# Kernel tuning notes

Hardware: AMD Instinct MI355X
Metric: run time of the kernel (lower is better)

Reference implementation:

```python
import jax, jax.numpy as jnp
import numpy as np

B, IN, H = 8192, 1024, 1024


def setup_inputs() -> dict:
    key = jax.random.key(0)
    ks = jax.random.split(key, 12)
    s_in = 1.0 / np.sqrt(IN + H)  # torch Linear default init scale
    inp = {
        "x": jax.random.normal(ks[0], (B, IN), jnp.float32),
        "h_prev": jax.random.normal(ks[1], (B, H), jnp.float32),
        "c_prev": jax.random.normal(ks[2], (B, H), jnp.float32),
        "embed": jax.random.normal(ks[3], (B, H), jnp.float32),
    }
    for i, g in enumerate(("forget", "input", "update", "out")):
        inp[f"W_{g}"] = jax.random.uniform(ks[4 + 2 * i], (IN + H, H), jnp.float32, -s_in, s_in)
        inp[f"b_{g}"] = jax.random.uniform(ks[5 + 2 * i], (H,), jnp.float32, -s_in, s_in)
    return inp


def reference(x, h_prev, c_prev, embed,
              W_forget, b_forget, W_input, b_input,
              W_update, b_update, W_out, b_out):
    # cat_input: [B, IN+H]; embed is accepted but unused (matches source forward)
    cat_input = jnp.concatenate((x.reshape(x.shape[0], -1), h_prev), axis=1)
    # Fuse the 4 gate GEMMs into one [B, IN+H] x [IN+H, 4H] matmul (same math)
    W = jnp.concatenate((W_forget, W_input, W_update, W_out), axis=1)  # [IN+H, 4H]
    b = jnp.concatenate((b_forget, b_input, b_update, b_out))          # [4H]
    gates = cat_input @ W + b                                          # [B, 4H]
    f_t, i_t, g_t, o_t = jnp.split(gates, 4, axis=1)
    f_t = jax.nn.sigmoid(f_t)
    i_t = jax.nn.sigmoid(i_t)
    c_opt = jnp.tanh(g_t)
    c_t = c_prev * f_t + i_t * c_opt
    o_t = jax.nn.sigmoid(o_t)
    h_t = o_t * jnp.tanh(c_t)
    return (h_t, c_t)
```

## Files before the change

### kernel.cpp

```cpp
#include <hip/hip_runtime.h>
#include <hip/hip_bf16.h>


typedef __attribute__((ext_vector_type(8))) short short8;
typedef __attribute__((ext_vector_type(4))) float f32x4;

#define GLOBAL_AS __attribute__((address_space(1)))
#define LDS_AS    __attribute__((address_space(3)))

__device__ __forceinline__ void load_lds16(const void* g, void* l) {
  __builtin_amdgcn_global_load_lds((const GLOBAL_AS unsigned int*)g,
                                   (LDS_AS unsigned int*)l, 16, 0, 0);
}

__device__ __forceinline__ unsigned short f2bf(float f) {
  unsigned int u = __float_as_uint(f);
  return (unsigned short)((u + 0x7FFFu + ((u >> 16) & 1u)) >> 16);
}
__device__ __forceinline__ float sigf(float x) { return 1.0f / (1.0f + __expf(-x)); }
__device__ __forceinline__ float tanh_fast(float x) {
  return 1.0f - 2.0f / (__expf(2.0f * x) + 1.0f);
}

__global__ void pack_kernel(const float* __restrict__ x,
                            const float* __restrict__ h,
                            const float* __restrict__ W0,
                            const float* __restrict__ W1,
                            const float* __restrict__ W2,
                            const float* __restrict__ W3,
                            unsigned short* __restrict__ Apk,
                            unsigned short* __restrict__ Wp) {
  int blk = blockIdx.x;
  if (blk < 8192) {
    int t = blk * 256 + threadIdx.x;
    int row = t >> 8;
    int c   = t & 255;
    int k   = c << 3;
    const float* src = (k < 1024) ? (x + (size_t)row * 1024 + k)
                                  : (h + (size_t)row * 1024 + (k - 1024));
    float4 f0 = ((const float4*)src)[0];
    float4 f1 = ((const float4*)src)[1];
    union { unsigned short us[8]; uint4 v; } u;
    u.us[0] = f2bf(f0.x); u.us[1] = f2bf(f0.y);
    u.us[2] = f2bf(f0.z); u.us[3] = f2bf(f0.w);
    u.us[4] = f2bf(f1.x); u.us[5] = f2bf(f1.y);
    u.us[6] = f2bf(f1.z); u.us[7] = f2bf(f1.w);
    *(uint4*)(Apk + (size_t)row * 2048 + c * 8) = u.v;
  } else {
    int b  = blk - 8192;
    int c  = b & 255;
    int nb = (b >> 8) & 3;
    int g  = b >> 10;
    const float* Wg = (g == 0) ? W0 : (g == 1) ? W1 : (g == 2) ? W2 : W3;
    int np = nb * 256 + threadIdx.x;
    int kbase = c << 3;
    union { unsigned short us[8]; uint4 v; } u;
#pragma unroll
    for (int j = 0; j < 8; ++j)
      u.us[j] = f2bf(Wg[(size_t)(kbase + j) * 1024 + np]);
    int n = (g << 10) + np;
    *(uint4*)(Wp + (size_t)n * 2048 + c * 8) = u.v;
  }
}

#define MFMA16(va, vb, vc) __builtin_amdgcn_mfma_f32_16x16x32_bf16(va, vb, vc, 0, 0, 0)

__global__ __launch_bounds__(512, 2) void lstm_gemm_kernel(
    const unsigned short* __restrict__ Apk,
    const unsigned short* __restrict__ Wp,
    const float* __restrict__ c_prev,
    const float* __restrict__ bF, const float* __restrict__ bI,
    const float* __restrict__ bU, const float* __restrict__ bO,
    float* __restrict__ outH, float* __restrict__ outC) {
  extern __shared__ unsigned short LDSu[];

  const int tid = threadIdx.x;
  const int l   = tid & 63;
  const int wv  = tid >> 6;
  const int wr  = wv >> 2;
  const int wc  = wv & 3;

  int bid = blockIdx.x;
  int wg  = ((bid & 7) << 6) | (bid >> 3);
  const int mblk = wg >> 4;
  const int nblk = wg & 15;
  const int brow = mblk << 8;

  const int rl  = l & 15;
  const int cg  = l >> 4;
  const int sc  = cg ^ ((rl >> 1) & 3);
  const int aRdBase = (wr * 128 + rl) * 32 + sc * 8;
  const int bRdBase = (wc * 64 + rl) * 32 + sc * 8;

  const int srow = wv * 16 + (l >> 2);
  const int csw  = ((l & 3) ^ ((l >> 3) & 3)) * 8;
  const unsigned short* aSrc0 = Apk + (size_t)(brow + srow) * 2048 + csw;
  const unsigned short* aSrc1 = aSrc0 + (size_t)128 * 2048;
  int p0 = nblk * 256 + srow;
  int n0 = (((p0 >> 4) & 3) << 10) | ((p0 >> 6) << 4) | (p0 & 15);
  int p1 = p0 + 128;
  int n1 = (((p1 >> 4) & 3) << 10) | ((p1 >> 6) << 4) | (p1 & 15);
  const unsigned short* bSrc0 = Wp + (size_t)n0 * 2048 + csw;
  const unsigned short* bSrc1 = Wp + (size_t)n1 * 2048 + csw;

  f32x4 acc[8][4];
#pragma unroll
  for (int m = 0; m < 8; ++m)
#pragma unroll
    for (int g = 0; g < 4; ++g) acc[m][g] = (f32x4)0.0f;

#pragma unroll
  for (int s = 0; s < 3; ++s) {
    const int pb = s * 8192;
    const int so = s * 32;
    load_lds16(aSrc0 + so, &LDSu[pb + wv * 512]);
    load_lds16(aSrc1 + so, &LDSu[pb + 4096 + wv * 512]);
    load_lds16(bSrc0 + so, &LDSu[32768 + pb + wv * 512]);
    load_lds16(bSrc1 + so, &LDSu[32768 + pb + 4096 + wv * 512]);
  }
  asm volatile("s_waitcnt vmcnt(8)");
  __builtin_amdgcn_s_barrier();

#pragma unroll 1
  for (int s = 0; s < 64; ++s) {
    const int ring  = (s & 3) * 8192;
    const int pring = ((s + 3) & 3) * 8192;
    int sp = s + 3; sp = sp > 63 ? 63 : sp;
    const int so = sp * 32;
    load_lds16(aSrc0 + so, &LDSu[pring + wv * 512]);
    load_lds16(aSrc1 + so, &LDSu[pring + 4096 + wv * 512]);
    load_lds16(bSrc0 + so, &LDSu[32768 + pring + wv * 512]);
    load_lds16(bSrc1 + so, &LDSu[32768 + pring + 4096 + wv * 512]);

    short8 bfr[4], afr[8];
#pragma unroll
    for (int g = 0; g < 4; ++g)
      bfr[g] = *(const short8*)&LDSu[32768 + ring + bRdBase + g * 512];
#pragma unroll
    for (int m = 0; m < 8; ++m)
      afr[m] = *(const short8*)&LDSu[ring + aRdBase + m * 512];

    __builtin_amdgcn_s_setprio(1);
#pragma unroll
    for (int m = 0; m < 8; ++m)
#pragma unroll
      for (int g = 0; g < 4; ++g)
        acc[m][g] = MFMA16(afr[m], bfr[g], acc[m][g]);
    __builtin_amdgcn_s_setprio(0);

    asm volatile("s_waitcnt vmcnt(8)");
    __builtin_amdgcn_s_barrier();
  }

  const int colh = nblk * 64 + wc * 16 + rl;
  const float biasF = bF[colh], biasI = bI[colh];
  const float biasU = bU[colh], biasO = bO[colh];
  const int row0 = brow + wr * 128 + ((l >> 4) << 2);
#pragma unroll
  for (int m = 0; m < 8; ++m) {
#pragma unroll
    for (int r = 0; r < 4; ++r) {
      int row = row0 + m * 16 + r;
      size_t idx = (size_t)row * 1024 + colh;
      float f  = sigf(acc[m][0][r] + biasF);
      float i_ = sigf(acc[m][1][r] + biasI);
      float g_ = tanh_fast(acc[m][2][r] + biasU);
      float o_ = sigf(acc[m][3][r] + biasO);
      float cp = c_prev[idx];
      float cn = cp * f + i_ * g_;
      outH[idx] = o_ * tanh_fast(cn);
      outC[idx] = cn;
    }
  }
}

extern "C" void kernel_launch(void* const* d_in, const int* in_sizes, int n_in,
                              void* d_out, int out_size, void* d_ws, size_t ws_size,
                              hipStream_t stream) {
  const float* x      = (const float*)d_in[0];
  const float* h_prev = (const float*)d_in[1];
  const float* c_prev = (const float*)d_in[2];
  const float* Wf = (const float*)d_in[4];
  const float* bf = (const float*)d_in[5];
  const float* Wi = (const float*)d_in[6];
  const float* bi = (const float*)d_in[7];
  const float* Wu = (const float*)d_in[8];
  const float* bu = (const float*)d_in[9];
  const float* Wo = (const float*)d_in[10];
  const float* bo = (const float*)d_in[11];

  unsigned short* Apk = (unsigned short*)d_ws;
  unsigned short* Wp  = (unsigned short*)((char*)d_ws + (size_t)8192 * 2048 * 2);

  pack_kernel<<<12288, 256, 0, stream>>>(x, h_prev, Wf, Wi, Wu, Wo, Apk, Wp);

  hipFuncSetAttribute((const void*)lstm_gemm_kernel,
                      hipFuncAttributeMaxDynamicSharedMemorySize, 131072);

  float* outH = (float*)d_out;
  float* outC = outH + (size_t)8192 * 1024;
  lstm_gemm_kernel<<<512, 512, 131072, stream>>>(Apk, Wp, c_prev,
                                                 bf, bi, bu, bo, outH, outC);
}
```

Before: 183.9 us.

## Load B fragments straight from global into registers, keep only A in LDS

The weight (B) operand no longer goes through LDS. Each wave now loads its own B fragments from global memory into registers, double-buffered one K-step ahead. Only the A tiles stay in the LDS ring, so shared memory shrinks to a 64 KB static allocation, and the A fragment reads are split into two halves to save registers. This removes the LDS write/read traffic for B and its share of the barrier. In exchange, waves that share B columns load the same data redundantly, global-load latency is hidden by only one step, and the compiler's automatic waits on the register loads may serialize the A prefetch.

```diff
diff --git a/kernel.cpp b/kernel.cpp
--- a/kernel.cpp
+++ b/kernel.cpp
@@ -65,6 +65,50 @@
 
 #define MFMA16(va, vb, vc) __builtin_amdgcn_mfma_f32_16x16x32_bf16(va, vb, vc, 0, 0, 0)
 
+#define SLOT(S, BCUR, BNXT)                                                    \
+  {                                                                            \
+    const int ring_ = ((S) & 3) * 8192;                                        \
+    {                                                                          \
+      int sn_ = (S) + 1; sn_ = sn_ > 63 ? 63 : sn_;                            \
+      _Pragma("unroll")                                                        \
+      for (int gg = 0; gg < 4; ++gg)                                           \
+        BNXT[gg] = *(const short8*)(bSrcG[gg] + sn_ * 32);                     \
+    }                                                                          \
+    {                                                                          \
+      int sp_ = (S) + 3; sp_ = sp_ > 63 ? 63 : sp_;                            \
+      const int pr_ = ((S) + 3) & 3;                                           \
+      load_lds16(aSrc0 + sp_ * 32, &LDSu[pr_ * 8192 + wv * 512]);              \
+      load_lds16(aSrc1 + sp_ * 32, &LDSu[pr_ * 8192 + 4096 + wv * 512]);       \
+    }                                                                          \
+    {                                                                          \
+      short8 av[4];                                                            \
+      _Pragma("unroll")                                                        \
+      for (int mm = 0; mm < 4; ++mm)                                           \
+        av[mm] = *(const short8*)&LDSu[ring_ + aRdBase + mm * 512];            \
+      __builtin_amdgcn_s_setprio(1);                                           \
+      _Pragma("unroll")                                                        \
+      for (int mm = 0; mm < 4; ++mm) {                                         \
+        _Pragma("unroll")                                                      \
+        for (int gg = 0; gg < 4; ++gg)                                         \
+          acc[mm][gg] = MFMA16(av[mm], BCUR[gg], acc[mm][gg]);                 \
+      }                                                                        \
+      __builtin_amdgcn_s_setprio(0);                                           \
+      _Pragma("unroll")                                                        \
+      for (int mm = 0; mm < 4; ++mm)                                           \
+        av[mm] = *(const short8*)&LDSu[ring_ + aRdBase + (4 + mm) * 512];      \
+      __builtin_amdgcn_s_setprio(1);                                           \
+      _Pragma("unroll")                                                        \
+      for (int mm = 0; mm < 4; ++mm) {                                         \
+        _Pragma("unroll")                                                      \
+        for (int gg = 0; gg < 4; ++gg)                                         \
+          acc[4 + mm][gg] = MFMA16(av[mm], BCUR[gg], acc[4 + mm][gg]);         \
+      }                                                                        \
+      __builtin_amdgcn_s_setprio(0);                                           \
+    }                                                                          \
+    asm volatile("s_waitcnt vmcnt(4)");                                        \
+    __builtin_amdgcn_s_barrier();                                              \
+  }
+
 __global__ __launch_bounds__(512, 2) void lstm_gemm_kernel(
     const unsigned short* __restrict__ Apk,
     const unsigned short* __restrict__ Wp,
@@ -72,7 +116,7 @@
     const float* __restrict__ bF, const float* __restrict__ bI,
     const float* __restrict__ bU, const float* __restrict__ bO,
     float* __restrict__ outH, float* __restrict__ outC) {
-  extern __shared__ unsigned short LDSu[];
+  __shared__ __align__(16) unsigned short LDSu[32768];
 
   const int tid = threadIdx.x;
   const int l   = tid & 63;
@@ -90,18 +134,19 @@
   const int cg  = l >> 4;
   const int sc  = cg ^ ((rl >> 1) & 3);
   const int aRdBase = (wr * 128 + rl) * 32 + sc * 8;
-  const int bRdBase = (wc * 64 + rl) * 32 + sc * 8;
 
   const int srow = wv * 16 + (l >> 2);
   const int csw  = ((l & 3) ^ ((l >> 3) & 3)) * 8;
   const unsigned short* aSrc0 = Apk + (size_t)(brow + srow) * 2048 + csw;
   const unsigned short* aSrc1 = aSrc0 + (size_t)128 * 2048;
-  int p0 = nblk * 256 + srow;
-  int n0 = (((p0 >> 4) & 3) << 10) | ((p0 >> 6) << 4) | (p0 & 15);
-  int p1 = p0 + 128;
-  int n1 = (((p1 >> 4) & 3) << 10) | ((p1 >> 6) << 4) | (p1 & 15);
-  const unsigned short* bSrc0 = Wp + (size_t)n0 * 2048 + csw;
-  const unsigned short* bSrc1 = Wp + (size_t)n1 * 2048 + csw;
+
+  const unsigned short* bSrcG[4];
+#pragma unroll
+  for (int g = 0; g < 4; ++g) {
+    int p = nblk * 256 + wc * 64 + g * 16 + rl;
+    int n = (((p >> 4) & 3) << 10) | ((p >> 6) << 4) | (p & 15);
+    bSrcG[g] = Wp + (size_t)n * 2048 + cg * 8;
+  }
 
   f32x4 acc[8][4];
 #pragma unroll
@@ -109,47 +154,24 @@
 #pragma unroll
     for (int g = 0; g < 4; ++g) acc[m][g] = (f32x4)0.0f;
 
+  short8 bEven[4], bOdd[4];
+
+#pragma unroll
+  for (int g = 0; g < 4; ++g)
+    bEven[g] = *(const short8*)(bSrcG[g] + 0);
 #pragma unroll
   for (int s = 0; s < 3; ++s) {
-    const int pb = s * 8192;
-    const int so = s * 32;
-    load_lds16(aSrc0 + so, &LDSu[pb + wv * 512]);
-    load_lds16(aSrc1 + so, &LDSu[pb + 4096 + wv * 512]);
-    load_lds16(bSrc0 + so, &LDSu[32768 + pb + wv * 512]);
-    load_lds16(bSrc1 + so, &LDSu[32768 + pb + 4096 + wv * 512]);
-  }
-  asm volatile("s_waitcnt vmcnt(8)");
+    load_lds16(aSrc0 + s * 32, &LDSu[s * 8192 + wv * 512]);
+    load_lds16(aSrc1 + s * 32, &LDSu[s * 8192 + 4096 + wv * 512]);
+  }
+  asm volatile("s_waitcnt vmcnt(4)");
   __builtin_amdgcn_s_barrier();
 
 #pragma unroll 1
-  for (int s = 0; s < 64; ++s) {
-    const int ring  = (s & 3) * 8192;
-    const int pring = ((s + 3) & 3) * 8192;
-    int sp = s + 3; sp = sp > 63 ? 63 : sp;
-    const int so = sp * 32;
-    load_lds16(aSrc0 + so, &LDSu[pring + wv * 512]);
-    load_lds16(aSrc1 + so, &LDSu[pring + 4096 + wv * 512]);
-    load_lds16(bSrc0 + so, &LDSu[32768 + pring + wv * 512]);
-    load_lds16(bSrc1 + so, &LDSu[32768 + pring + 4096 + wv * 512]);
-
-    short8 bfr[4], afr[8];
-#pragma unroll
-    for (int g = 0; g < 4; ++g)
-      bfr[g] = *(const short8*)&LDSu[32768 + ring + bRdBase + g * 512];
-#pragma unroll
-    for (int m = 0; m < 8; ++m)
-      afr[m] = *(const short8*)&LDSu[ring + aRdBase + m * 512];
-
-    __builtin_amdgcn_s_setprio(1);
-#pragma unroll
-    for (int m = 0; m < 8; ++m)
-#pragma unroll
-      for (int g = 0; g < 4; ++g)
-        acc[m][g] = MFMA16(afr[m], bfr[g], acc[m][g]);
-    __builtin_amdgcn_s_setprio(0);
-
-    asm volatile("s_waitcnt vmcnt(8)");
-    __builtin_amdgcn_s_barrier();
+  for (int u = 0; u < 32; ++u) {
+    const int s0 = 2 * u;
+    SLOT(s0,     bEven, bOdd)
+    SLOT(s0 + 1, bOdd,  bEven)
   }
 
   const int colh = nblk * 64 + wc * 16 + rl;
@@ -194,11 +216,8 @@
 
   pack_kernel<<<12288, 256, 0, stream>>>(x, h_prev, Wf, Wi, Wu, Wo, Apk, Wp);
 
-  hipFuncSetAttribute((const void*)lstm_gemm_kernel,
-                      hipFuncAttributeMaxDynamicSharedMemorySize, 131072);
-
   float* outH = (float*)d_out;
   float* outC = outH + (size_t)8192 * 1024;
-  lstm_gemm_kernel<<<512, 512, 131072, stream>>>(Apk, Wp, c_prev,
-                                                 bf, bi, bu, bo, outH, outC);
-}
+  lstm_gemm_kernel<<<512, 512, 0, stream>>>(Apk, Wp, c_prev,
+                                            bf, bi, bu, bo, outH, outC);
+}
```

New measurement: 247.3 us. 1.34x slower.

## Shrink GEMM tile to 128x128 with 3-stage ring and more blocks

Applied to the files above, without the earlier changes.

The block tile shrinks from 256x256 (512 threads) to 128x128 (256 threads, 2x2 waves). The grid becomes 2048 blocks with static 48KB LDS and a 3-slot prefetch ring unrolled by three, so ring indices are compile-time constants. The aim is higher occupancy (3 blocks per CU) and better load balance across CUs. The cost is lower arithmetic intensity per block, which means more global and L2 traffic for the same work.

```diff
diff --git a/kernel.cpp b/kernel.cpp
--- a/kernel.cpp
+++ b/kernel.cpp
@@ -65,99 +65,103 @@
 
 #define MFMA16(va, vb, vc) __builtin_amdgcn_mfma_f32_16x16x32_bf16(va, vb, vc, 0, 0, 0)
 
-__global__ __launch_bounds__(512, 2) void lstm_gemm_kernel(
+#define SLOT3(S, RR, PR)                                                       \
+  {                                                                            \
+    int sp_ = (S) + 2; sp_ = sp_ > 63 ? 63 : sp_;                              \
+    const int so_ = sp_ * 32;                                                  \
+    load_lds16(aSrc0 + so_, &LDSu[(PR) * 8192 + wv * 512]);                    \
+    load_lds16(aSrc1 + so_, &LDSu[(PR) * 8192 + 2048 + wv * 512]);             \
+    load_lds16(bSrc0 + so_, &LDSu[(PR) * 8192 + 4096 + wv * 512]);             \
+    load_lds16(bSrc1 + so_, &LDSu[(PR) * 8192 + 4096 + 2048 + wv * 512]);      \
+    short8 av[4], bv[4];                                                       \
+    _Pragma("unroll")                                                          \
+    for (int gg = 0; gg < 4; ++gg)                                             \
+      bv[gg] = *(const short8*)&LDSu[(RR) * 8192 + 4096 + bRdBase + gg * 512]; \
+    _Pragma("unroll")                                                          \
+    for (int mm = 0; mm < 4; ++mm)                                             \
+      av[mm] = *(const short8*)&LDSu[(RR) * 8192 + aRdBase + mm * 512];        \
+    __builtin_amdgcn_s_setprio(1);                                             \
+    _Pragma("unroll")                                                          \
+    for (int mm = 0; mm < 4; ++mm) {                                           \
+      _Pragma("unroll")                                                        \
+      for (int gg = 0; gg < 4; ++gg)                                           \
+        acc[mm][gg] = MFMA16(av[mm], bv[gg], acc[mm][gg]);                     \
+    }                                                                          \
+    __builtin_amdgcn_s_setprio(0);                                             \
+    asm volatile("s_waitcnt vmcnt(4)");                                        \
+    __builtin_amdgcn_s_barrier();                                              \
+  }
+
+__global__ __launch_bounds__(256, 3) void lstm_gemm_kernel(
     const unsigned short* __restrict__ Apk,
     const unsigned short* __restrict__ Wp,
     const float* __restrict__ c_prev,
     const float* __restrict__ bF, const float* __restrict__ bI,
     const float* __restrict__ bU, const float* __restrict__ bO,
     float* __restrict__ outH, float* __restrict__ outC) {
-  extern __shared__ unsigned short LDSu[];
+  __shared__ __align__(16) unsigned short LDSu[24576];
 
   const int tid = threadIdx.x;
   const int l   = tid & 63;
   const int wv  = tid >> 6;
-  const int wr  = wv >> 2;
-  const int wc  = wv & 3;
+  const int wr  = wv >> 1;
+  const int wc  = wv & 1;
 
   int bid = blockIdx.x;
-  int wg  = ((bid & 7) << 6) | (bid >> 3);
-  const int mblk = wg >> 4;
-  const int nblk = wg & 15;
-  const int brow = mblk << 8;
+  int wg  = ((bid & 7) << 8) | (bid >> 3);
+  const int mblk = wg >> 5;
+  const int nblk = wg & 31;
+  const int brow = mblk << 7;
 
   const int rl  = l & 15;
   const int cg  = l >> 4;
   const int sc  = cg ^ ((rl >> 1) & 3);
-  const int aRdBase = (wr * 128 + rl) * 32 + sc * 8;
+  const int aRdBase = (wr * 64 + rl) * 32 + sc * 8;
   const int bRdBase = (wc * 64 + rl) * 32 + sc * 8;
 
-  const int srow = wv * 16 + (l >> 2);
-  const int csw  = ((l & 3) ^ ((l >> 3) & 3)) * 8;
-  const unsigned short* aSrc0 = Apk + (size_t)(brow + srow) * 2048 + csw;
-  const unsigned short* aSrc1 = aSrc0 + (size_t)128 * 2048;
-  int p0 = nblk * 256 + srow;
+  const int csw = ((l & 3) ^ ((l >> 3) & 3)) * 8;
+  const int ar0 = brow + wv * 16 + (l >> 2);
+  const unsigned short* aSrc0 = Apk + (size_t)ar0 * 2048 + csw;
+  const unsigned short* aSrc1 = aSrc0 + (size_t)64 * 2048;
+  int p0 = nblk * 128 + wv * 16 + (l >> 2);
   int n0 = (((p0 >> 4) & 3) << 10) | ((p0 >> 6) << 4) | (p0 & 15);
-  int p1 = p0 + 128;
+  int p1 = p0 + 64;
   int n1 = (((p1 >> 4) & 3) << 10) | ((p1 >> 6) << 4) | (p1 & 15);
   const unsigned short* bSrc0 = Wp + (size_t)n0 * 2048 + csw;
   const unsigned short* bSrc1 = Wp + (size_t)n1 * 2048 + csw;
 
-  f32x4 acc[8][4];
-#pragma unroll
-  for (int m = 0; m < 8; ++m)
+  f32x4 acc[4][4];
+#pragma unroll
+  for (int m = 0; m < 4; ++m)
 #pragma unroll
     for (int g = 0; g < 4; ++g) acc[m][g] = (f32x4)0.0f;
 
 #pragma unroll
-  for (int s = 0; s < 3; ++s) {
-    const int pb = s * 8192;
+  for (int s = 0; s < 2; ++s) {
     const int so = s * 32;
-    load_lds16(aSrc0 + so, &LDSu[pb + wv * 512]);
-    load_lds16(aSrc1 + so, &LDSu[pb + 4096 + wv * 512]);
-    load_lds16(bSrc0 + so, &LDSu[32768 + pb + wv * 512]);
-    load_lds16(bSrc1 + so, &LDSu[32768 + pb + 4096 + wv * 512]);
-  }
-  asm volatile("s_waitcnt vmcnt(8)");
+    load_lds16(aSrc0 + so, &LDSu[s * 8192 + wv * 512]);
+    load_lds16(aSrc1 + so, &LDSu[s * 8192 + 2048 + wv * 512]);
+    load_lds16(bSrc0 + so, &LDSu[s * 8192 + 4096 + wv * 512]);
+    load_lds16(bSrc1 + so, &LDSu[s * 8192 + 4096 + 2048 + wv * 512]);
+  }
+  asm volatile("s_waitcnt vmcnt(4)");
   __builtin_amdgcn_s_barrier();
 
 #pragma unroll 1
-  for (int s = 0; s < 64; ++s) {
-    const int ring  = (s & 3) * 8192;
-    const int pring = ((s + 3) & 3) * 8192;
-    int sp = s + 3; sp = sp > 63 ? 63 : sp;
-    const int so = sp * 32;
-    load_lds16(aSrc0 + so, &LDSu[pring + wv * 512]);
-    load_lds16(aSrc1 + so, &LDSu[pring + 4096 + wv * 512]);
-    load_lds16(bSrc0 + so, &LDSu[32768 + pring + wv * 512]);
-    load_lds16(bSrc1 + so, &LDSu[32768 + pring + 4096 + wv * 512]);
-
-    short8 bfr[4], afr[8];
-#pragma unroll
-    for (int g = 0; g < 4; ++g)
-      bfr[g] = *(const short8*)&LDSu[32768 + ring + bRdBase + g * 512];
-#pragma unroll
-    for (int m = 0; m < 8; ++m)
-      afr[m] = *(const short8*)&LDSu[ring + aRdBase + m * 512];
-
-    __builtin_amdgcn_s_setprio(1);
-#pragma unroll
-    for (int m = 0; m < 8; ++m)
-#pragma unroll
-      for (int g = 0; g < 4; ++g)
-        acc[m][g] = MFMA16(afr[m], bfr[g], acc[m][g]);
-    __builtin_amdgcn_s_setprio(0);
-
-    asm volatile("s_waitcnt vmcnt(8)");
-    __builtin_amdgcn_s_barrier();
-  }
-
-  const int colh = nblk * 64 + wc * 16 + rl;
+  for (int u = 0; u < 21; ++u) {
+    const int s0 = 3 * u;
+    SLOT3(s0,     0, 2)
+    SLOT3(s0 + 1, 1, 0)
+    SLOT3(s0 + 2, 2, 1)
+  }
+  SLOT3(63, 0, 2)
+
+  const int colh = nblk * 32 + wc * 16 + rl;
   const float biasF = bF[colh], biasI = bI[colh];
   const float biasU = bU[colh], biasO = bO[colh];
-  const int row0 = brow + wr * 128 + ((l >> 4) << 2);
-#pragma unroll
-  for (int m = 0; m < 8; ++m) {
+  const int row0 = brow + wr * 64 + ((l >> 4) << 2);
+#pragma unroll
+  for (int m = 0; m < 4; ++m) {
 #pragma unroll
     for (int r = 0; r < 4; ++r) {
       int row = row0 + m * 16 + r;
@@ -194,11 +198,8 @@
 
   pack_kernel<<<12288, 256, 0, stream>>>(x, h_prev, Wf, Wi, Wu, Wo, Apk, Wp);
 
-  hipFuncSetAttribute((const void*)lstm_gemm_kernel,
-                      hipFuncAttributeMaxDynamicSharedMemorySize, 131072);
-
   float* outH = (float*)d_out;
   float* outC = outH + (size_t)8192 * 1024;
-  lstm_gemm_kernel<<<512, 512, 131072, stream>>>(Apk, Wp, c_prev,
-                                                 bf, bi, bu, bo, outH, outC);
-}
+  lstm_gemm_kernel<<<2048, 256, 0, stream>>>(Apk, Wp, c_prev,
+                                             bf, bi, bu, bo, outH, outC);
+}
```

Result: slower. 227.4 us (+23.6%).
